# Performance work log

Measured on AMD Instinct MI355X. Metric: run time of the kernel, lower is better.

Reference implementation:

```python
import jax, jax.numpy as jnp
import numpy as np

TS = 1.0  # simulation time step (Ts from network.yaml)


def alpha_psp(x, tau):
    """SLAYER psp: causal temporal conv of x (time-major, (T,...)) with the
    SRM alpha kernel eps[k] = (k*Ts/tau)*exp(1 - k*Ts/tau), scaled by Ts.
    eps[k] = (Ts*e/tau) * k * d**k with d = exp(-Ts/tau), realized exactly by a
    2-state linear recurrence instead of an O(T^2) FIR."""
    d = jnp.asarray(np.exp(-TS / tau), x.dtype)
    c = jnp.asarray(np.e * TS / tau * TS, x.dtype)  # kernel amp * Ts integration

    def step(carry, x_t):
        u, v = carry                       # u = sum x_s d^(t-1-s); v = sum x_s (t-1-s) d^(t-1-s)
        v_new = d * (v + u)                # -> sum_{s<=t} x_s (t-s) d^(t-s)  (x_t weight 0)
        u_new = d * u + x_t
        return (u_new, v_new), c * v_new

    z = jnp.zeros_like(x[0])
    _, out = jax.lax.scan(step, (z, z), x)
    return out


def lif_spike(u_in, theta, tauRef, scaleRef):
    """SLAYER spike function: sequential threshold over time with alpha-shaped
    refractory response nu[k] = -scaleRef*theta*(k*Ts/tauRef)*exp(1-k*Ts/tauRef)
    added after every spike. Same 2-state recurrence generates the refractory
    sum exactly. u_in is time-major (T, ...). Spike amplitude is 1/Ts."""
    d = jnp.asarray(np.exp(-TS / tauRef), u_in.dtype)
    c = jnp.asarray(-scaleRef * theta * np.e * TS / tauRef, u_in.dtype)

    def step(carry, u_t):
        u, v = carry
        v_new = d * (v + u)                # refractory state from past spikes only
        m = u_t + c * v_new                # membrane potential incl. refractory
        s = (m >= theta).astype(u_t.dtype)
        return (d * u + s, v_new), (s / TS, m)

    z = jnp.zeros_like(u_in[0])
    _, (spikes, membrane) = jax.lax.scan(step, (z, z), u_in)
    return spikes, membrane


def conv2d_t(x, w, pad):
    """Per-time-step 2D conv (SLAYER conv3d with time-kernel 1, no bias).
    x: (T, N, C, H, W), w: (O, I, kh, kw)."""
    T, N, C, H, W = x.shape
    y = jax.lax.conv_general_dilated(
        x.reshape(T * N, C, H, W), w, (1, 1), [(pad, pad), (pad, pad)],
        dimension_numbers=('NCHW', 'OIHW', 'NCHW'))
    return y.reshape(T, N, -1, H, W)


def setup_inputs() -> dict:
    key = jax.random.key(0)
    k1, k2, k3 = jax.random.split(key, 3)
    # binary event spike train, (N, C, H, W, T)
    spikeInput = (jax.random.uniform(k1, (4, 1, 192, 192, 64)) < 0.2).astype(jnp.float32)
    # SLAYER conv weights (bias=False); scaled up (weightScale~100 in SLAYER)
    W1 = jax.random.normal(k2, (1, 1, 5, 5), jnp.float32) * 10.0
    W2 = jax.random.normal(k3, (1, 1, 3, 3), jnp.float32) * 10.0
    return {"spikeInput": spikeInput, "W1": W1, "W2": W2}


def reference(spikeInput, W1, W2):
    x = jnp.moveaxis(spikeInput, -1, 0)          # (T, N, C, H, W) time-major
    psp1 = alpha_psp(x, tau=1.0)                 # slayer1.psp (tauSr=1)
    s1, _ = lif_spike(conv2d_t(psp1, W1, 2), theta=30.0, tauRef=1.0, scaleRef=1.0)
    psp2 = alpha_psp(s1, tau=2.0)                # slayer2.psp (tauSr=2)
    s2, _ = lif_spike(conv2d_t(psp2, W2, 1), theta=50.0, tauRef=2.0, scaleRef=1.0)
    return jnp.moveaxis(s2, 0, -1)               # back to (N, C, H, W, T)
```

## Files before the change

kernel.cpp:

```cpp
#include <hip/hip_runtime.h>


#define HH   192
#define WW   192
#define NIMG 4
#define TT   64
#define NT   256
#define XW   6
#define XH   12

#define E_D 2.718281828459045
static constexpr float D1  = (float)0.36787944117144233;
static constexpr float CP1 = (float)(E_D);
static constexpr float DR1 = (float)0.36787944117144233;
static constexpr float CR1 = (float)(-30.0 * E_D);
static constexpr float D2  = (float)0.6065306597126334;
static constexpr float CP2 = (float)(E_D * 0.5);
static constexpr float DR2 = (float)0.6065306597126334;
static constexpr float CR2 = (float)(-50.0 * E_D * 0.5);
static constexpr float TH1 = 30.0f;
static constexpr float TH2 = 50.0f;

__global__ __launch_bounds__(NT)
void ka_pack(const float* __restrict__ in, unsigned* __restrict__ bitT) {
    const int gw = blockIdx.x * (NT / 64) + (threadIdx.x >> 6);
    const int ln = threadIdx.x & 63;
    const int xw = gw % XW;
    const int ny = gw / XW;
    const float* src = in + ((size_t)ny * WW + xw * 32) * TT + ln;
    unsigned w = 0u;
#pragma unroll
    for (int x = 0; x < 32; x++) {
        const float v = src[(size_t)x * TT];
        w |= (v != 0.f) ? (1u << x) : 0u;
    }
    bitT[((size_t)ny * XW + xw) * TT + ln] = w;
}

__global__ __launch_bounds__(NT, 8)
void l1_convscan(const unsigned* __restrict__ bitT, const float* __restrict__ w1g,
                 unsigned short* __restrict__ s1h) {
    __shared__ float ct[64 * 65];
    __shared__ uint2 tb[64];

    const int n = blockIdx.z, ys = blockIdx.y, xs = blockIdx.x;
    const int y0 = ys * 4, x0 = xs * 16;
    const int tid = threadIdx.x;
    const int wv = tid >> 6, ln = tid & 63;

    float w1r[25];
#pragma unroll
    for (int k = 0; k < 25; k++) w1r[k] = w1g[k];

    const int a = (x0 - 2) >> 5;
    const int s = (x0 - 2) & 31;
    const int gyb = y0 + wv;
    unsigned w20[5];
#pragma unroll
    for (int dy = 0; dy < 5; dy++) {
        const int gy = gyb - 2 + dy;
        unsigned wa = 0u, wb = 0u;
        if (gy >= 0 && gy < HH) {
            const unsigned* rp = bitT + ((size_t)(n * HH + gy) * XW) * TT + ln;
            if (a >= 0)     wa = rp[(size_t)a * TT];
            if (a + 1 < XW) wb = rp[(size_t)(a + 1) * TT];
        }
        w20[dy] = (wa >> s) | (wb << (32 - s));
    }

#pragma unroll
    for (int col = 0; col < 16; col++) {
        float l0 = 0.f, l1 = 0.f, l2 = 0.f, l3 = 0.f, l4 = 0.f;
#pragma unroll
        for (int j = 0; j < 5; j++) {
            l0 += (float)((w20[0] >> (col + j)) & 1u) * w1r[j];
            l1 += (float)((w20[1] >> (col + j)) & 1u) * w1r[5 + j];
            l2 += (float)((w20[2] >> (col + j)) & 1u) * w1r[10 + j];
            l3 += (float)((w20[3] >> (col + j)) & 1u) * w1r[15 + j];
            l4 += (float)((w20[4] >> (col + j)) & 1u) * w1r[20 + j];
        }
        ct[(wv * 16 + col) * 65 + ln] = ((l0 + l1) + (l2 + l3)) + l4;
    }
    __syncthreads();

    if (tid < 64) {
        const int px = tid;
        float u1 = 0.f, v1 = 0.f, ur = 0.f, vr = 0.f;
        unsigned slo = 0u, shi = 0u;
#pragma unroll
        for (int tc = 0; tc < TT; tc += 8) {
            float c8[8];
#pragma unroll
            for (int j = 0; j < 8; j++) c8[j] = ct[px * 65 + tc + j];
#pragma unroll
            for (int j = 0; j < 8; j++) {
                v1 = D1 * (v1 + u1);
                const float p = CP1 * v1;
                u1 = D1 * u1 + c8[j];
                vr = DR1 * (vr + ur);
                const float m = p + CR1 * vr;
                const bool sp = (m >= TH1);
                ur = DR1 * ur + (sp ? 1.f : 0.f);
                const unsigned bit = sp ? (1u << ((tc + j) & 31)) : 0u;
                if (tc < 32) slo |= bit;
                else         shi |= bit;
            }
        }
        tb[px] = make_uint2(slo, shi);
    }
    __syncthreads();

    {
        unsigned h = 0u;
#pragma unroll
        for (int x = 0; x < 16; x++) {
            const uint2 b = tb[wv * 16 + x];
            const unsigned w = (ln < 32) ? b.x : b.y;
            h |= ((w >> (ln & 31)) & 1u) << x;
        }
        s1h[((size_t)(n * HH + gyb) * XH + xs) * TT + ln] = (unsigned short)h;
    }
}

__global__ __launch_bounds__(NT, 8)
void l2_convscan(const unsigned short* __restrict__ s1h, const float* __restrict__ w2g,
                 float* __restrict__ out) {
    __shared__ float          lut3[512];
    __shared__ unsigned short ptile[64 * 66];
    __shared__ uint2          tb[64];

    const int n = blockIdx.z, ys = blockIdx.y, xs = blockIdx.x;
    const int y0 = ys * 4;
    const int tid = threadIdx.x;
    const int wv = tid >> 6, ln = tid & 63;

#pragma unroll
    for (int e = tid; e < 512; e += NT) {
        float l0 = 0.f, l1 = 0.f, l2 = 0.f;
#pragma unroll
        for (int j = 0; j < 3; j++) {
            if ((e >> j) & 1)       l0 += w2g[j];
            if ((e >> (3 + j)) & 1) l1 += w2g[3 + j];
            if ((e >> (6 + j)) & 1) l2 += w2g[6 + j];
        }
        lut3[e] = (l0 + l1) + l2;
    }

    const int gyb = y0 + wv;
    unsigned w18[3];
#pragma unroll
    for (int dy = 0; dy < 3; dy++) {
        const int gy = gyb - 1 + dy;
        unsigned hm = 0u, h0 = 0u, hp = 0u;
        if (gy >= 0 && gy < HH) {
            const unsigned short* rp = s1h + ((size_t)(n * HH + gy) * XH) * TT + ln;
            if (xs > 0)      hm = rp[(size_t)(xs - 1) * TT];
            h0 = rp[(size_t)xs * TT];
            if (xs + 1 < XH) hp = rp[(size_t)(xs + 1) * TT];
        }
        w18[dy] = (hm >> 15) | (h0 << 1) | ((hp & 1u) << 17);
    }
    __syncthreads();

#pragma unroll
    for (int col = 0; col < 16; col++) {
        const unsigned pat = ((w18[0] >> col) & 7)
                           | (((w18[1] >> col) & 7) << 3)
                           | (((w18[2] >> col) & 7) << 6);
        ptile[(wv * 16 + col) * 66 + ln] = (unsigned short)pat;
    }
    __syncthreads();

    if (tid < 64) {
        const int px = tid;
        const unsigned* pp = (const unsigned*)(ptile + px * 66);
        float u2 = 0.f, v2 = 0.f, ur2 = 0.f, vr2 = 0.f;
        unsigned olo = 0u, ohi = 0u;
#pragma unroll
        for (int tc = 0; tc < TT; tc += 8) {
            unsigned q[4];
#pragma unroll
            for (int k = 0; k < 4; k++) q[k] = pp[tc / 2 + k];
            float l[8];
#pragma unroll
            for (int k = 0; k < 4; k++) {
                l[2 * k + 0] = lut3[q[k] & 0x1ffu];
                l[2 * k + 1] = lut3[(q[k] >> 16) & 0x1ffu];
            }
#pragma unroll
            for (int j = 0; j < 8; j++) {
                v2 = D2 * (v2 + u2);
                const float p = CP2 * v2;
                u2 = D2 * u2 + l[j];
                vr2 = DR2 * (vr2 + ur2);
                const float m = p + CR2 * vr2;
                const bool sp = (m >= TH2);
                ur2 = DR2 * ur2 + (sp ? 1.f : 0.f);
                const unsigned bit = sp ? (1u << ((tc + j) & 31)) : 0u;
                if (tc < 32) olo |= bit;
                else         ohi |= bit;
            }
        }
        tb[px] = make_uint2(olo, ohi);
    }
    __syncthreads();

    const int sh = ln & 31;
#pragma unroll
    for (int k = 0; k < 16; k++) {
        const uint2 b = tb[wv * 16 + k];
        const unsigned w = (ln < 32) ? b.x : b.y;
        out[((size_t)(n * HH + gyb) * WW + xs * 16 + k) * TT + ln] =
            (float)((w >> sh) & 1u);
    }
}

extern "C" void kernel_launch(void* const* d_in, const int* in_sizes, int n_in,
                              void* d_out, int out_size, void* d_ws, size_t ws_size,
                              hipStream_t stream) {
    const float* in = (const float*)d_in[0];
    const float* w1 = (const float*)d_in[1];
    const float* w2 = (const float*)d_in[2];
    float* out = (float*)d_out;

    char* ws = (char*)d_ws;
    unsigned*       bitT = (unsigned*)ws;
    unsigned short* s1h  = (unsigned short*)(ws + (2ull << 20));

    const int ka_blocks = (NIMG * HH * XW) / (NT / 64);
    dim3 cgrid(WW / 16, HH / 4, NIMG);
    ka_pack    <<<ka_blocks, NT, 0, stream>>>(in, bitT);
    l1_convscan<<<cgrid, NT, 0, stream>>>(bitT, w1, s1h);
    l2_convscan<<<cgrid, NT, 0, stream>>>(s1h, w2, out);
}
```

Before: 117.1 us.

## Give every wave its own scan tile so all 256 threads run recurrences

Result: slower. 119.5 us (+2.1%).

```diff
diff --git a/kernel.cpp b/kernel.cpp
--- a/kernel.cpp
+++ b/kernel.cpp
@@ -37,28 +37,33 @@
     bitT[((size_t)ny * XW + xw) * TT + ln] = w;
 }
 
-__global__ __launch_bounds__(NT, 8)
+__global__ __launch_bounds__(NT, 2)
 void l1_convscan(const unsigned* __restrict__ bitT, const float* __restrict__ w1g,
                  unsigned short* __restrict__ s1h) {
-    __shared__ float ct[64 * 65];
-    __shared__ uint2 tb[64];
+    __shared__ float ct[4][64 * 65];
+    __shared__ uint2 tb[4][64];
 
     const int n = blockIdx.z, ys = blockIdx.y, xs = blockIdx.x;
-    const int y0 = ys * 4, x0 = xs * 16;
+    const int y0 = ys * 16, x0 = xs * 16;
     const int tid = threadIdx.x;
     const int wv = tid >> 6, ln = tid & 63;
+    const int yb = y0 + wv * 4;
 
     float w1r[25];
 #pragma unroll
-    for (int k = 0; k < 25; k++) w1r[k] = w1g[k];
+    for (int k = 0; k < 25; k++) {
+        union { float f; int i; } u;
+        u.f = w1g[k];
+        u.i = __builtin_amdgcn_readfirstlane(u.i);
+        w1r[k] = u.f;
+    }
 
     const int a = (x0 - 2) >> 5;
     const int s = (x0 - 2) & 31;
-    const int gyb = y0 + wv;
-    unsigned w20[5];
-#pragma unroll
-    for (int dy = 0; dy < 5; dy++) {
-        const int gy = gyb - 2 + dy;
+    unsigned w20[8];
+#pragma unroll
+    for (int dy = 0; dy < 8; dy++) {
+        const int gy = yb - 2 + dy;
         unsigned wa = 0u, wb = 0u;
         if (gy >= 0 && gy < HH) {
             const unsigned* rp = bitT + ((size_t)(n * HH + gy) * XW) * TT + ln;
@@ -69,29 +74,46 @@
     }
 
 #pragma unroll
-    for (int col = 0; col < 16; col++) {
-        float l0 = 0.f, l1 = 0.f, l2 = 0.f, l3 = 0.f, l4 = 0.f;
-#pragma unroll
-        for (int j = 0; j < 5; j++) {
-            l0 += (float)((w20[0] >> (col + j)) & 1u) * w1r[j];
-            l1 += (float)((w20[1] >> (col + j)) & 1u) * w1r[5 + j];
-            l2 += (float)((w20[2] >> (col + j)) & 1u) * w1r[10 + j];
-            l3 += (float)((w20[3] >> (col + j)) & 1u) * w1r[15 + j];
-            l4 += (float)((w20[4] >> (col + j)) & 1u) * w1r[20 + j];
-        }
-        ct[(wv * 16 + col) * 65 + ln] = ((l0 + l1) + (l2 + l3)) + l4;
-    }
-    __syncthreads();
-
-    if (tid < 64) {
-        const int px = tid;
+    for (int h = 0; h < 2; h++) {
+        const int ch = h * 8;
+        float b[8][12];
+#pragma unroll
+        for (int k = 0; k < 8; k++)
+#pragma unroll
+            for (int c = 0; c < 12; c++)
+                b[k][c] = (float)((w20[k] >> (ch + c)) & 1u);
+#pragma unroll
+        for (int r = 0; r < 4; r++) {
+#pragma unroll
+            for (int col = 0; col < 8; col++) {
+                float l0 = b[r + 0][col] * w1r[0];
+                float l1 = b[r + 1][col] * w1r[5];
+                float l2 = b[r + 2][col] * w1r[10];
+                float l3 = b[r + 3][col] * w1r[15];
+                float l4 = b[r + 4][col] * w1r[20];
+#pragma unroll
+                for (int j = 1; j < 5; j++) {
+                    l0 += b[r + 0][col + j] * w1r[j];
+                    l1 += b[r + 1][col + j] * w1r[5 + j];
+                    l2 += b[r + 2][col + j] * w1r[10 + j];
+                    l3 += b[r + 3][col + j] * w1r[15 + j];
+                    l4 += b[r + 4][col + j] * w1r[20 + j];
+                }
+                ct[wv][(r * 16 + ch + col) * 65 + ln] = ((l0 + l1) + (l2 + l3)) + l4;
+            }
+        }
+    }
+    __syncthreads();
+
+    {
+        const int px = ln;
         float u1 = 0.f, v1 = 0.f, ur = 0.f, vr = 0.f;
         unsigned slo = 0u, shi = 0u;
 #pragma unroll
         for (int tc = 0; tc < TT; tc += 8) {
             float c8[8];
 #pragma unroll
-            for (int j = 0; j < 8; j++) c8[j] = ct[px * 65 + tc + j];
+            for (int j = 0; j < 8; j++) c8[j] = ct[wv][px * 65 + tc + j];
 #pragma unroll
             for (int j = 0; j < 8; j++) {
                 v1 = D1 * (v1 + u1);
@@ -106,33 +128,35 @@
                 else         shi |= bit;
             }
         }
-        tb[px] = make_uint2(slo, shi);
-    }
-    __syncthreads();
-
-    {
+        tb[wv][px] = make_uint2(slo, shi);
+    }
+    __syncthreads();
+
+#pragma unroll
+    for (int r = 0; r < 4; r++) {
         unsigned h = 0u;
 #pragma unroll
         for (int x = 0; x < 16; x++) {
-            const uint2 b = tb[wv * 16 + x];
-            const unsigned w = (ln < 32) ? b.x : b.y;
+            const uint2 bb = tb[wv][r * 16 + x];
+            const unsigned w = (ln < 32) ? bb.x : bb.y;
             h |= ((w >> (ln & 31)) & 1u) << x;
         }
-        s1h[((size_t)(n * HH + gyb) * XH + xs) * TT + ln] = (unsigned short)h;
-    }
-}
-
-__global__ __launch_bounds__(NT, 8)
+        s1h[((size_t)(n * HH + yb + r) * XH + xs) * TT + ln] = (unsigned short)h;
+    }
+}
+
+__global__ __launch_bounds__(NT, 4)
 void l2_convscan(const unsigned short* __restrict__ s1h, const float* __restrict__ w2g,
                  float* __restrict__ out) {
     __shared__ float          lut3[512];
-    __shared__ unsigned short ptile[64 * 66];
-    __shared__ uint2          tb[64];
+    __shared__ unsigned short ptile[4][64 * 66];
+    __shared__ uint2          tb[4][64];
 
     const int n = blockIdx.z, ys = blockIdx.y, xs = blockIdx.x;
-    const int y0 = ys * 4;
+    const int y0 = ys * 16;
     const int tid = threadIdx.x;
     const int wv = tid >> 6, ln = tid & 63;
+    const int yb = y0 + wv * 4;
 
 #pragma unroll
     for (int e = tid; e < 512; e += NT) {
@@ -146,11 +170,10 @@
         lut3[e] = (l0 + l1) + l2;
     }
 
-    const int gyb = y0 + wv;
-    unsigned w18[3];
-#pragma unroll
-    for (int dy = 0; dy < 3; dy++) {
-        const int gy = gyb - 1 + dy;
+    unsigned w18[6];
+#pragma unroll
+    for (int dy = 0; dy < 6; dy++) {
+        const int gy = yb - 1 + dy;
         unsigned hm = 0u, h0 = 0u, hp = 0u;
         if (gy >= 0 && gy < HH) {
             const unsigned short* rp = s1h + ((size_t)(n * HH + gy) * XH) * TT + ln;
@@ -163,17 +186,19 @@
     __syncthreads();
 
 #pragma unroll
-    for (int col = 0; col < 16; col++) {
-        const unsigned pat = ((w18[0] >> col) & 7)
-                           | (((w18[1] >> col) & 7) << 3)
-                           | (((w18[2] >> col) & 7) << 6);
-        ptile[(wv * 16 + col) * 66 + ln] = (unsigned short)pat;
-    }
-    __syncthreads();
-
-    if (tid < 64) {
-        const int px = tid;
-        const unsigned* pp = (const unsigned*)(ptile + px * 66);
+    for (int r = 0; r < 4; r++)
+#pragma unroll
+        for (int col = 0; col < 16; col++) {
+            const unsigned pat = ((w18[r + 0] >> col) & 7)
+                               | (((w18[r + 1] >> col) & 7) << 3)
+                               | (((w18[r + 2] >> col) & 7) << 6);
+            ptile[wv][(r * 16 + col) * 66 + ln] = (unsigned short)pat;
+        }
+    __syncthreads();
+
+    {
+        const int px = ln;
+        const unsigned* pp = (const unsigned*)(&ptile[wv][px * 66]);
         float u2 = 0.f, v2 = 0.f, ur2 = 0.f, vr2 = 0.f;
         unsigned olo = 0u, ohi = 0u;
 #pragma unroll
@@ -201,18 +226,20 @@
                 else         ohi |= bit;
             }
         }
-        tb[px] = make_uint2(olo, ohi);
+        tb[wv][px] = make_uint2(olo, ohi);
     }
     __syncthreads();
 
     const int sh = ln & 31;
 #pragma unroll
-    for (int k = 0; k < 16; k++) {
-        const uint2 b = tb[wv * 16 + k];
-        const unsigned w = (ln < 32) ? b.x : b.y;
-        out[((size_t)(n * HH + gyb) * WW + xs * 16 + k) * TT + ln] =
-            (float)((w >> sh) & 1u);
-    }
+    for (int r = 0; r < 4; r++)
+#pragma unroll
+        for (int k = 0; k < 16; k++) {
+            const uint2 bb = tb[wv][r * 16 + k];
+            const unsigned w = (ln < 32) ? bb.x : bb.y;
+            out[((size_t)(n * HH + yb + r) * WW + xs * 16 + k) * TT + ln] =
+                (float)((w >> sh) & 1u);
+        }
 }
 
 extern "C" void kernel_launch(void* const* d_in, const int* in_sizes, int n_in,
@@ -228,7 +255,7 @@
     unsigned short* s1h  = (unsigned short*)(ws + (2ull << 20));
 
     const int ka_blocks = (NIMG * HH * XW) / (NT / 64);
-    dim3 cgrid(WW / 16, HH / 4, NIMG);
+    dim3 cgrid(WW / 16, HH / 16, NIMG);
     ka_pack    <<<ka_blocks, NT, 0, stream>>>(in, bitT);
     l1_convscan<<<cgrid, NT, 0, stream>>>(bitT, w1, s1h);
     l2_convscan<<<cgrid, NT, 0, stream>>>(s1h, w2, out);
```
